# Performance work log

Hardware: AMD Instinct MI355X
Metric: run time of the kernel (lower is better)

The kernel has to match this reference:

```python
import jax, jax.numpy as jnp
import numpy as np

D_MODEL = 2048
N_HEADS = 16
HEAD_DIM = 128
WINDOW = 512
ROPE_BASE = 10000.0
B, N = 2, 2048
INNER = N_HEADS * HEAD_DIM


def setup_inputs() -> dict:
    key = jax.random.key(0)
    k1, k2, k3 = jax.random.split(key, 3)
    x = jax.random.normal(k1, (B, N, D_MODEL), dtype=jnp.float32)
    # torch nn.Linear stores weight as [out_features, in_features]
    w_qkv = jax.random.normal(k2, (3 * INNER, D_MODEL), dtype=jnp.float32) / np.sqrt(D_MODEL)
    w_o = jax.random.normal(k3, (D_MODEL, INNER), dtype=jnp.float32) / np.sqrt(INNER)
    return {"x": x, "w_qkv": w_qkv, "w_o": w_o}


def _rotate_half(t):
    t1, t2 = jnp.split(t, 2, axis=-1)
    return jnp.concatenate([-t2, t1], axis=-1)


def _rope(q, k, offset=0):
    # q, k: [B, H, N, D]; GPT-NeoX half-split rotary embedding
    D = q.shape[-1]
    inv_freq = 1.0 / (ROPE_BASE ** (jnp.arange(0, D, 2, dtype=jnp.float32) / D))
    pos = jnp.arange(q.shape[2], dtype=jnp.float32) + offset
    ang = pos[:, None] * inv_freq[None, :]                 # [N, D/2]
    cos = jnp.concatenate([jnp.cos(ang), jnp.cos(ang)], axis=-1)  # [N, D]
    sin = jnp.concatenate([jnp.sin(ang), jnp.sin(ang)], axis=-1)
    q_r = q * cos + _rotate_half(q) * sin
    k_r = k * cos + _rotate_half(k) * sin
    return q_r, k_r


def reference(x, w_qkv, w_o):
    Bq, Nq, _ = x.shape
    # QKV projection (no bias)
    qkv = jnp.einsum('bnd,ed->bne', x, w_qkv)              # [B, N, 3*INNER]
    q, k, v = jnp.split(qkv, 3, axis=-1)
    def to_heads(t):
        return t.reshape(Bq, Nq, N_HEADS, HEAD_DIM).transpose(0, 2, 1, 3)  # [B,H,N,D]
    q, k, v = to_heads(q), to_heads(k), to_heads(v)
    q, k = _rope(q, k, offset=0)
    # sliding-window causal mask: valid key j for query i iff (i - WINDOW) < j <= i
    i = jnp.arange(Nq)[:, None]
    j = jnp.arange(Nq)[None, :]
    valid = (j > i - WINDOW) & (j <= i)                    # [N, N]
    scale = 1.0 / np.sqrt(HEAD_DIM)
    scores = jnp.einsum('bhnd,bhkd->bhnk', q, k) * scale   # [B,H,N,N]
    scores = jnp.where(valid[None, None], scores, -jnp.inf)
    att = jax.nn.softmax(scores, axis=-1)
    out = jnp.einsum('bhnk,bhkd->bhnd', att, v)
    out = out.transpose(0, 2, 1, 3).reshape(Bq, Nq, INNER)
    y = jnp.einsum('bni,di->bnd', out, w_o)
    return y
```

## Files before the change

### kernel.cpp

```cpp
#include <hip/hip_runtime.h>
#include <hip/hip_bf16.h>
#include <cstdint>

typedef __bf16 bf16x8 __attribute__((ext_vector_type(8)));
typedef float floatx4 __attribute__((ext_vector_type(4)));

__device__ __forceinline__ void gl2lds16(const void* g, void* l) {
  __builtin_amdgcn_global_load_lds(
      (const __attribute__((address_space(1))) unsigned int*)g,
      (__attribute__((address_space(3))) unsigned int*)(uintptr_t)l,
      16, 0, 0);
}

__global__ __launch_bounds__(256)
void cvt_kernel(const float* __restrict__ in, __hip_bfloat16* __restrict__ out, int n) {
  int i = (blockIdx.x * 256 + threadIdx.x) * 4;
  if (i >= n) return;
  const float4 v = *(const float4*)(in + i);
  out[i + 0] = __float2bfloat16(v.x);
  out[i + 1] = __float2bfloat16(v.y);
  out[i + 2] = __float2bfloat16(v.z);
  out[i + 3] = __float2bfloat16(v.w);
}

__global__ __launch_bounds__(256)
void cvt2_kernel(const float* __restrict__ in0, const float* __restrict__ in1,
                 __hip_bfloat16* __restrict__ out, int n0, int ntot) {
  int i = (blockIdx.x * 256 + threadIdx.x) * 4;
  if (i >= ntot) return;
  const float4 v = (i < n0) ? *(const float4*)(in0 + i)
                            : *(const float4*)(in1 + (i - n0));
  out[i + 0] = __float2bfloat16(v.x);
  out[i + 1] = __float2bfloat16(v.y);
  out[i + 2] = __float2bfloat16(v.z);
  out[i + 3] = __float2bfloat16(v.w);
}

#define MEMFENCE asm volatile("" ::: "memory")

__global__ __launch_bounds__(256, 3)
void gemm_qkv128(const __hip_bfloat16* __restrict__ A,
                 const __hip_bfloat16* __restrict__ W,
                 __hip_bfloat16* __restrict__ Qr,
                 __hip_bfloat16* __restrict__ Kr,
                 __hip_bfloat16* __restrict__ Vt)
{
  extern __shared__ __hip_bfloat16 sm[];
  const int tid = threadIdx.x, lane = tid & 63, wave = tid >> 6;
  const int wr = wave >> 1, wc = wave & 1;
  const int bid = blockIdx.y * 32 + blockIdx.x;
  const int swz = (bid & 7) * 192 + (bid >> 3);
  const int m0 = (swz & 31) << 7;
  const int n0 = (swz >> 5) << 7;
  const int lrow = lane & 15, dg = lane >> 4, lq4 = dg * 4;
  const int rslot = (dg ^ ((lrow >> 1) & 3)) * 8;
  const int arow = tid >> 2;
  const int ascol = ((tid & 3) ^ ((tid >> 3) & 3)) * 8;
  const __hip_bfloat16* aS0 = A + (size_t)(m0 + arow) * 2048 + ascol;
  const __hip_bfloat16* aS1 = A + (size_t)(m0 + 64 + arow) * 2048 + ascol;
  const __hip_bfloat16* bS0 = W + (size_t)(n0 + arow) * 2048 + ascol;
  const __hip_bfloat16* bS1 = W + (size_t)(n0 + 64 + arow) * 2048 + ascol;
  float* invfp = (float*)((char*)sm + 49152);
  if (tid < 64) invfp[tid] = __expf(-(float)tid * 0.14391156831212787f);
  floatx4 acc[4][4] = {};

#define QS128(TT) do { const int bo_ = ((TT) % 3) * 8192; const int kk_ = (TT) * 32; \
    gl2lds16(aS0 + kk_, &sm[bo_ + tid * 8]);                                   \
    gl2lds16(aS1 + kk_, &sm[bo_ + 2048 + tid * 8]);                            \
    gl2lds16(bS0 + kk_, &sm[bo_ + 4096 + tid * 8]);                            \
    gl2lds16(bS1 + kk_, &sm[bo_ + 6144 + tid * 8]); } while (0)

#define QC128(BO) do {                                                         \
    bf16x8 af[4], bfr[4];                                                      \
    _Pragma("unroll")                                                          \
    for (int mt = 0; mt < 4; mt++)                                             \
      af[mt] = *(const bf16x8*)&sm[(BO) + (wr * 64 + mt * 16 + lrow) * 32 + rslot]; \
    _Pragma("unroll")                                                          \
    for (int nt = 0; nt < 4; nt++)                                             \
      bfr[nt] = *(const bf16x8*)&sm[(BO) + 4096 + (wc * 64 + nt * 16 + lrow) * 32 + rslot]; \
    __builtin_amdgcn_s_setprio(1);                                             \
    _Pragma("unroll")                                                          \
    for (int mt = 0; mt < 4; mt++)                                             \
      _Pragma("unroll")                                                        \
      for (int nt = 0; nt < 4; nt++)                                           \
        acc[mt][nt] = __builtin_amdgcn_mfma_f32_16x16x32_bf16(af[mt], bfr[nt], acc[mt][nt], 0, 0, 0); \
    __builtin_amdgcn_s_setprio(0);                                             \
  } while (0)

  QS128(0); QS128(1);
  for (int t = 0; t < 63; ++t) {
    MEMFENCE; __builtin_amdgcn_s_waitcnt(0x0074); MEMFENCE;
    __builtin_amdgcn_s_barrier(); MEMFENCE;
    if (t < 62) QS128(t + 2);
    QC128((t % 3) * 8192);
  }
  MEMFENCE; __builtin_amdgcn_s_waitcnt(0x0070); MEMFENCE;
  __builtin_amdgcn_s_barrier(); MEMFENCE;
  QC128((63 % 3) * 8192);
#undef QC128
#undef QS128

  const int seg = n0 >> 11;
  const int h = (n0 & 2047) >> 7;
  const int b = m0 >> 11;
  const int seq0 = m0 & 2047;
  __syncthreads();
  if (seg < 2) {
#pragma unroll
    for (int mt = 0; mt < 4; mt++)
#pragma unroll
      for (int nt = 0; nt < 4; nt++)
#pragma unroll
        for (int r = 0; r < 4; r++)
          sm[(wr * 64 + mt * 16 + lq4 + r) * 136 + wc * 64 + nt * 16 + lrow] =
              __float2bfloat16(acc[mt][nt][r]);
  } else {
#pragma unroll
    for (int mt = 0; mt < 4; mt++)
#pragma unroll
      for (int nt = 0; nt < 4; nt++)
#pragma unroll
        for (int r = 0; r < 4; r++)
          sm[(wc * 64 + nt * 16 + lrow) * 136 + wr * 64 + mt * 16 + lq4 + r] =
              __float2bfloat16(acc[mt][nt][r]);
  }
  __syncthreads();
  const float qs = (seg == 0) ? 0.08838834764831845f : 1.0f;
  if (seg < 2) {
    __hip_bfloat16* Out = seg ? Kr : Qr;
#pragma unroll
    for (int it = 0; it < 4; ++it) {
      const int task = tid + it * 256;
      const int row = task >> 3;
      const int g8 = (task & 7) * 8;
      const int seq = seq0 + row;
      const float pos = (float)seq;
      const bf16x8 lo8 = *(const bf16x8*)&sm[row * 136 + g8];
      const bf16x8 hi8 = *(const bf16x8*)&sm[row * 136 + g8 + 64];
      alignas(16) __hip_bfloat16 lo[8], hi[8];
#pragma unroll
      for (int k = 0; k < 8; k++) {
        float sn, cs;
        __sincosf(pos * invfp[g8 + k], &sn, &cs);
        const float a = (float)lo8[k];
        const float bb2 = (float)hi8[k];
        lo[k] = __float2bfloat16((a * cs - bb2 * sn) * qs);
        hi[k] = __float2bfloat16((bb2 * cs + a * sn) * qs);
      }
      const size_t ob = ((size_t)((b * 16 + h) * 2048 + seq)) * 128;
      *(bf16x8*)&Out[ob + g8] = *(const bf16x8*)lo;
      *(bf16x8*)&Out[ob + g8 + 64] = *(const bf16x8*)hi;
    }
  } else {
#pragma unroll
    for (int it = 0; it < 8; ++it) {
      const int task = tid + it * 256;
      const int col = task >> 4;
      const int sg = (task & 15) * 8;
      const bf16x8 v8 = *(const bf16x8*)&sm[col * 136 + sg];
      *(bf16x8*)&Vt[((size_t)((b * 16 + h) * 128 + col)) * 2048 + seq0 + sg] = v8;
    }
  }
}

__global__ __launch_bounds__(512, 2)
void gemm_o256(const __hip_bfloat16* __restrict__ A,
               const __hip_bfloat16* __restrict__ Wo,
               float* __restrict__ C)
{
  extern __shared__ __hip_bfloat16 sm[];
  const int tid = threadIdx.x, lane = tid & 63, wave = tid >> 6;
  const int wr = wave >> 2, wc = wave & 3;
  const int m0 = blockIdx.x << 8, n0 = blockIdx.y << 7;
  const int lrow = lane & 15, dg = lane >> 4, lq4 = dg * 4;
  const int rslot = (dg ^ ((lrow >> 1) & 3)) * 8;
  const int arow = tid >> 2;
  const int ascol = ((tid & 3) ^ ((tid >> 3) & 3)) * 8;
  const __hip_bfloat16* aS0 = A + (size_t)(m0 + arow) * 2048 + ascol;
  const __hip_bfloat16* aS1 = A + (size_t)(m0 + 128 + arow) * 2048 + ascol;
  const __hip_bfloat16* bS0 = Wo + (size_t)(n0 + arow) * 2048 + ascol;
  floatx4 acc[8][2] = {};

#define OSTAGE(TT) do { const int bb_ = (TT) & 3; const int kk_ = (TT) * 32;   \
    gl2lds16(aS0 + kk_, &sm[bb_ * 12288 + tid * 8]);                           \
    gl2lds16(aS1 + kk_, &sm[bb_ * 12288 + 4096 + tid * 8]);                    \
    gl2lds16(bS0 + kk_, &sm[bb_ * 12288 + 8192 + tid * 8]); } while (0)

#define OKSTEP(TT, WIMM, DOSTAGE) do {                                         \
    MEMFENCE; __builtin_amdgcn_s_waitcnt(WIMM); MEMFENCE;                      \
    __builtin_amdgcn_s_barrier(); MEMFENCE;                                    \
    const int bb = (TT) & 3;                                                   \
    if (DOSTAGE) OSTAGE((TT) + 3);                                             \
    bf16x8 af[8], bfr[2];                                                      \
    _Pragma("unroll")                                                          \
    for (int mt = 0; mt < 8; mt++)                                             \
      af[mt] = *(const bf16x8*)&sm[bb * 12288 + (wr * 128 + mt * 16 + lrow) * 32 + rslot]; \
    _Pragma("unroll")                                                          \
    for (int nt = 0; nt < 2; nt++)                                             \
      bfr[nt] = *(const bf16x8*)&sm[bb * 12288 + 8192 + (wc * 32 + nt * 16 + lrow) * 32 + rslot]; \
    __builtin_amdgcn_s_setprio(1);                                             \
    _Pragma("unroll")                                                          \
    for (int mt = 0; mt < 8; mt++)                                             \
      _Pragma("unroll")                                                        \
      for (int nt = 0; nt < 2; nt++)                                           \
        acc[mt][nt] = __builtin_amdgcn_mfma_f32_16x16x32_bf16(af[mt], bfr[nt], acc[mt][nt], 0, 0, 0); \
    __builtin_amdgcn_s_setprio(0);                                             \
  } while (0)

  OSTAGE(0); OSTAGE(1); OSTAGE(2);
  for (int t = 0; t < 61; ++t) OKSTEP(t, 0x0076, true);
  OKSTEP(61, 0x0076, false);
  OKSTEP(62, 0x0073, false);
  OKSTEP(63, 0x0070, false);
#undef OKSTEP
#undef OSTAGE

#pragma unroll
  for (int mt = 0; mt < 8; mt++)
#pragma unroll
    for (int nt = 0; nt < 2; nt++)
#pragma unroll
      for (int r = 0; r < 4; r++)
        C[(size_t)(m0 + wr * 128 + mt * 16 + lq4 + r) * 2048 +
          (n0 + wc * 32 + nt * 16 + lrow)] = acc[mt][nt][r];
}

#define KSTR 136
#define VSTR 72
__global__ __launch_bounds__(512, 4)
void attn_swa(const __hip_bfloat16* __restrict__ Qr, const __hip_bfloat16* __restrict__ Kr,
              const __hip_bfloat16* __restrict__ Vt, __hip_bfloat16* __restrict__ Out)
{
  __shared__ __hip_bfloat16 Ks[64 * KSTR];
  __shared__ __hip_bfloat16 Vs[128 * VSTR];
  __shared__ __hip_bfloat16 Pb[8][16 * VSTR];
  const int qt = blockIdx.x, bh = blockIdx.y;
  const int tid = threadIdx.x, lane = tid & 63, wave = tid >> 6;
  const int lrow = lane & 15, lk = (lane >> 4) * 8, lq4 = (lane >> 4) * 4;
  const int i0 = qt * 128;
  const float NEG_INF = -__builtin_inff();
  const __hip_bfloat16* Qh = Qr + (size_t)bh * 2048 * 128;
  const __hip_bfloat16* Kh = Kr + (size_t)bh * 2048 * 128;
  const __hip_bfloat16* Vh = Vt + (size_t)bh * 128 * 2048;

  const int ck0 = tid, ck1 = tid + 512;
  const int kr0 = ck0 >> 4, kg0 = (ck0 & 15) * 8;
  const int kr1 = ck1 >> 4, kg1 = (ck1 & 15) * 8;
  const int cv0 = tid, cv1 = tid + 512;
  const int vd0 = cv0 >> 3, vc0 = (cv0 & 7) * 8;
  const int vd1 = cv1 >> 3, vc1 = (cv1 & 7) * 8;

  const int iw = i0 + wave * 16 + lrow;
  bf16x8 qf[4];
#pragma unroll
  for (int ks = 0; ks < 4; ks++)
    qf[ks] = *(const bf16x8*)&Qh[(size_t)iw * 128 + ks * 32 + lk];

  floatx4 accO[8] = {};
  float m_i = NEG_INF, l_i = 0.f;
  const int imin = i0 + wave * 16;
  const int lo = i0 - 511;
  const int jt_lo = (lo > 0 ? lo : 0) >> 6;
  const int jt_hi = (i0 + 127) >> 6;

  int j0n = jt_lo * 64;
  int4 rk0 = *(const int4*)&Kh[(size_t)(j0n + kr0) * 128 + kg0];
  int4 rk1 = *(const int4*)&Kh[(size_t)(j0n + kr1) * 128 + kg1];
  int4 rv0 = *(const int4*)&Vh[(size_t)vd0 * 2048 + j0n + vc0];
  int4 rv1 = *(const int4*)&Vh[(size_t)vd1 * 2048 + j0n + vc1];

  for (int jt = jt_lo; jt <= jt_hi; jt++) {
    const int j0 = jt * 64;
    __syncthreads();
    *(int4*)&Ks[kr0 * KSTR + kg0] = rk0;
    *(int4*)&Ks[kr1 * KSTR + kg1] = rk1;
    *(int4*)&Vs[vd0 * VSTR + vc0] = rv0;
    *(int4*)&Vs[vd1 * VSTR + vc1] = rv1;
    if (jt < jt_hi) {
      const int jn = j0 + 64;
      rk0 = *(const int4*)&Kh[(size_t)(jn + kr0) * 128 + kg0];
      rk1 = *(const int4*)&Kh[(size_t)(jn + kr1) * 128 + kg1];
      rv0 = *(const int4*)&Vh[(size_t)vd0 * 2048 + jn + vc0];
      rv1 = *(const int4*)&Vh[(size_t)vd1 * 2048 + jn + vc1];
    }
    asm volatile("" ::: "memory");
    __builtin_amdgcn_s_waitcnt(0xC07F);
    __builtin_amdgcn_s_barrier();
    asm volatile("" ::: "memory");

    floatx4 s[4] = {};
#pragma unroll
    for (int nt = 0; nt < 4; nt++) {
      const int krow = (nt * 16 + lrow) * KSTR;
#pragma unroll
      for (int ks = 0; ks < 4; ks++) {
        const bf16x8 kf = *(const bf16x8*)&Ks[krow + ks * 32 + lk];
        s[nt] = __builtin_amdgcn_mfma_f32_16x16x32_bf16(kf, qf[ks], s[nt], 0, 0, 0);
      }
    }
    const bool full = (j0 + 63 <= imin) && (j0 >= imin + 15 - 511);
    float rmax = NEG_INF;
    if (full) {
#pragma unroll
      for (int nt = 0; nt < 4; nt++)
#pragma unroll
        for (int r = 0; r < 4; r++) rmax = fmaxf(rmax, s[nt][r]);
    } else {
#pragma unroll
      for (int nt = 0; nt < 4; nt++) {
#pragma unroll
        for (int r = 0; r < 4; r++) {
          const int j = j0 + nt * 16 + lq4 + r;
          const float sv = ((j <= iw) && (j > iw - 512)) ? s[nt][r] : NEG_INF;
          s[nt][r] = sv;
          rmax = fmaxf(rmax, sv);
        }
      }
    }
    rmax = fmaxf(rmax, __shfl_xor(rmax, 16));
    rmax = fmaxf(rmax, __shfl_xor(rmax, 32));
    const float mnew = fmaxf(m_i, rmax);
    const float alpha = __expf(fminf(m_i - mnew, 0.f));
    m_i = mnew;
    float rs = 0.f;
    if (full) {
#pragma unroll
      for (int nt = 0; nt < 4; nt++)
#pragma unroll
        for (int r = 0; r < 4; r++) {
          const float p = __expf(s[nt][r] - mnew);
          s[nt][r] = p;
          rs += p;
        }
    } else {
#pragma unroll
      for (int nt = 0; nt < 4; nt++)
#pragma unroll
        for (int r = 0; r < 4; r++) {
          const float sv = s[nt][r];
          const float p = (sv == NEG_INF) ? 0.f : __expf(sv - mnew);
          s[nt][r] = p;
          rs += p;
        }
    }
    rs += __shfl_xor(rs, 16);
    rs += __shfl_xor(rs, 32);
    l_i = l_i * alpha + rs;
#pragma unroll
    for (int dt = 0; dt < 8; dt++) accO[dt] *= alpha;
#pragma unroll
    for (int nt = 0; nt < 4; nt++) {
      alignas(8) __hip_bfloat16 p4[4];
#pragma unroll
      for (int r = 0; r < 4; r++) p4[r] = __float2bfloat16(s[nt][r]);
      *(uint64_t*)&Pb[wave][lrow * VSTR + nt * 16 + lq4] = *(const uint64_t*)p4;
    }
    bf16x8 pf[2];
#pragma unroll
    for (int jf = 0; jf < 2; jf++)
      pf[jf] = *(const bf16x8*)&Pb[wave][lrow * VSTR + jf * 32 + lk];
#pragma unroll
    for (int dt = 0; dt < 8; dt++) {
      const int vrow = (dt * 16 + lrow) * VSTR;
#pragma unroll
      for (int jf = 0; jf < 2; jf++) {
        const bf16x8 vf = *(const bf16x8*)&Vs[vrow + jf * 32 + lk];
        accO[dt] = __builtin_amdgcn_mfma_f32_16x16x32_bf16(vf, pf[jf], accO[dt], 0, 0, 0);
      }
    }
  }
  const int b = bh >> 4, h = bh & 15;
  const float inv_l = 1.0f / l_i;
  const size_t rowb = ((size_t)(b * 2048 + iw)) * 2048 + h * 128;
#pragma unroll
  for (int dt = 0; dt < 8; dt++) {
    alignas(8) __hip_bfloat16 o4[4];
#pragma unroll
    for (int r = 0; r < 4; r++) o4[r] = __float2bfloat16(accO[dt][r] * inv_l);
    *(uint64_t*)&Out[rowb + dt * 16 + lq4] = *(const uint64_t*)o4;
  }
}

extern "C" void kernel_launch(void* const* d_in, const int* in_sizes, int n_in,
                              void* d_out, int out_size, void* d_ws, size_t ws_size,
                              hipStream_t stream)
{
  const float* x = (const float*)d_in[0];
  const float* w_qkv = (const float*)d_in[1];
  const float* w_o = (const float*)d_in[2];
  float* y = (float*)d_out;
  char* ws = (char*)d_ws;

  const size_t SZ_X = 16777216;
  const size_t SZ_WQKV = 25165824;
  const size_t SZ_Q = 16777216;

  __hip_bfloat16* xb = (__hip_bfloat16*)(ws);
  __hip_bfloat16* wqkvb = (__hip_bfloat16*)(ws + SZ_X);
  __hip_bfloat16* Qr = (__hip_bfloat16*)(ws + SZ_X + SZ_WQKV);
  __hip_bfloat16* Kr = (__hip_bfloat16*)(ws + SZ_X + SZ_WQKV + SZ_Q);
  __hip_bfloat16* Vt = (__hip_bfloat16*)(ws + SZ_X + SZ_WQKV + 2 * SZ_Q);

  static bool s_attr_done = false;
  if (!s_attr_done) {
    hipFuncSetAttribute((const void*)gemm_o256,
                        hipFuncAttributeMaxDynamicSharedMemorySize, 98304);
    s_attr_done = true;
  }

  cvt2_kernel<<<dim3(20480), dim3(256), 0, stream>>>(x, w_qkv, xb, 8388608, 20971520);
  gemm_qkv128<<<dim3(32, 48), dim3(256), 49408, stream>>>(xb, wqkvb, Qr, Kr, Vt);
  attn_swa<<<dim3(16, 32), dim3(512), 0, stream>>>(Qr, Kr, Vt, xb );
  cvt_kernel<<<dim3(4096), dim3(256), 0, stream>>>(w_o, wqkvb, 4194304);
  gemm_o256<<<dim3(16, 16), dim3(512), 98304, stream>>>(xb, wqkvb, y);
}
```

Measured before the change: 357.9 us.

## Enlarge QKV GEMM tile to 256x128 with 512-thread blocks

Reworks the QKV projection GEMM from 128x128 tiles on 256 threads to 256x128 tiles on 512 threads (8 waves arranged 4x2). The LDS staging buffers, the load pattern, the grid swizzle and the epilogue transpose strides are all updated to match. Each block now reuses every weight tile across twice as many rows, which cuts global and L2 traffic for W. The cost is more shared memory per block (about 74KB) and a grid of half as many blocks, which may reduce occupancy and tail balance.

```diff
diff --git a/kernel.cpp b/kernel.cpp
--- a/kernel.cpp
+++ b/kernel.cpp
@@ -38,46 +38,44 @@
 
 #define MEMFENCE asm volatile("" ::: "memory")
 
-__global__ __launch_bounds__(256, 3)
-void gemm_qkv128(const __hip_bfloat16* __restrict__ A,
-                 const __hip_bfloat16* __restrict__ W,
-                 __hip_bfloat16* __restrict__ Qr,
-                 __hip_bfloat16* __restrict__ Kr,
-                 __hip_bfloat16* __restrict__ Vt)
+__global__ __launch_bounds__(512, 4)
+void gemm_qkvA(const __hip_bfloat16* __restrict__ A,
+               const __hip_bfloat16* __restrict__ W,
+               __hip_bfloat16* __restrict__ Qr,
+               __hip_bfloat16* __restrict__ Kr,
+               __hip_bfloat16* __restrict__ Vt)
 {
   extern __shared__ __hip_bfloat16 sm[];
   const int tid = threadIdx.x, lane = tid & 63, wave = tid >> 6;
   const int wr = wave >> 1, wc = wave & 1;
-  const int bid = blockIdx.y * 32 + blockIdx.x;
-  const int swz = (bid & 7) * 192 + (bid >> 3);
-  const int m0 = (swz & 31) << 7;
-  const int n0 = (swz >> 5) << 7;
+  const int idx = blockIdx.y * 16 + blockIdx.x;
+  const int swz = (idx & 7) * 96 + (idx >> 3);
+  const int m0 = (swz & 15) << 8;
+  const int n0 = (swz >> 4) << 7;
   const int lrow = lane & 15, dg = lane >> 4, lq4 = dg * 4;
   const int rslot = (dg ^ ((lrow >> 1) & 3)) * 8;
   const int arow = tid >> 2;
   const int ascol = ((tid & 3) ^ ((tid >> 3) & 3)) * 8;
   const __hip_bfloat16* aS0 = A + (size_t)(m0 + arow) * 2048 + ascol;
-  const __hip_bfloat16* aS1 = A + (size_t)(m0 + 64 + arow) * 2048 + ascol;
+  const __hip_bfloat16* aS1 = A + (size_t)(m0 + 128 + arow) * 2048 + ascol;
   const __hip_bfloat16* bS0 = W + (size_t)(n0 + arow) * 2048 + ascol;
-  const __hip_bfloat16* bS1 = W + (size_t)(n0 + 64 + arow) * 2048 + ascol;
-  float* invfp = (float*)((char*)sm + 49152);
+  float* invfp = (float*)((char*)sm + 73728);
   if (tid < 64) invfp[tid] = __expf(-(float)tid * 0.14391156831212787f);
   floatx4 acc[4][4] = {};
 
-#define QS128(TT) do { const int bo_ = ((TT) % 3) * 8192; const int kk_ = (TT) * 32; \
+#define ASTG(TT) do { const int bo_ = ((TT) % 3) * 12288; const int kk_ = (TT) * 32; \
     gl2lds16(aS0 + kk_, &sm[bo_ + tid * 8]);                                   \
-    gl2lds16(aS1 + kk_, &sm[bo_ + 2048 + tid * 8]);                            \
-    gl2lds16(bS0 + kk_, &sm[bo_ + 4096 + tid * 8]);                            \
-    gl2lds16(bS1 + kk_, &sm[bo_ + 6144 + tid * 8]); } while (0)
-
-#define QC128(BO) do {                                                         \
+    gl2lds16(aS1 + kk_, &sm[bo_ + 4096 + tid * 8]);                            \
+    gl2lds16(bS0 + kk_, &sm[bo_ + 8192 + tid * 8]); } while (0)
+
+#define ACOMP(BO) do {                                                         \
     bf16x8 af[4], bfr[4];                                                      \
     _Pragma("unroll")                                                          \
     for (int mt = 0; mt < 4; mt++)                                             \
       af[mt] = *(const bf16x8*)&sm[(BO) + (wr * 64 + mt * 16 + lrow) * 32 + rslot]; \
     _Pragma("unroll")                                                          \
     for (int nt = 0; nt < 4; nt++)                                             \
-      bfr[nt] = *(const bf16x8*)&sm[(BO) + 4096 + (wc * 64 + nt * 16 + lrow) * 32 + rslot]; \
+      bfr[nt] = *(const bf16x8*)&sm[(BO) + 8192 + (wc * 64 + nt * 16 + lrow) * 32 + rslot]; \
     __builtin_amdgcn_s_setprio(1);                                             \
     _Pragma("unroll")                                                          \
     for (int mt = 0; mt < 4; mt++)                                             \
@@ -87,18 +85,18 @@
     __builtin_amdgcn_s_setprio(0);                                             \
   } while (0)
 
-  QS128(0); QS128(1);
+  ASTG(0); ASTG(1);
   for (int t = 0; t < 63; ++t) {
-    MEMFENCE; __builtin_amdgcn_s_waitcnt(0x0074); MEMFENCE;
+    MEMFENCE; __builtin_amdgcn_s_waitcnt(0x0073); MEMFENCE;
     __builtin_amdgcn_s_barrier(); MEMFENCE;
-    if (t < 62) QS128(t + 2);
-    QC128((t % 3) * 8192);
+    if (t < 62) ASTG(t + 2);
+    ACOMP((t % 3) * 12288);
   }
   MEMFENCE; __builtin_amdgcn_s_waitcnt(0x0070); MEMFENCE;
   __builtin_amdgcn_s_barrier(); MEMFENCE;
-  QC128((63 % 3) * 8192);
-#undef QC128
-#undef QS128
+  ACOMP((63 % 3) * 12288);
+#undef ACOMP
+#undef ASTG
 
   const int seg = n0 >> 11;
   const int h = (n0 & 2047) >> 7;
@@ -121,7 +119,7 @@
       for (int nt = 0; nt < 4; nt++)
 #pragma unroll
         for (int r = 0; r < 4; r++)
-          sm[(wc * 64 + nt * 16 + lrow) * 136 + wr * 64 + mt * 16 + lq4 + r] =
+          sm[(wc * 64 + nt * 16 + lrow) * 264 + wr * 64 + mt * 16 + lq4 + r] =
               __float2bfloat16(acc[mt][nt][r]);
   }
   __syncthreads();
@@ -130,7 +128,7 @@
     __hip_bfloat16* Out = seg ? Kr : Qr;
 #pragma unroll
     for (int it = 0; it < 4; ++it) {
-      const int task = tid + it * 256;
+      const int task = tid + it * 512;
       const int row = task >> 3;
       const int g8 = (task & 7) * 8;
       const int seq = seq0 + row;
@@ -154,10 +152,10 @@
   } else {
 #pragma unroll
     for (int it = 0; it < 8; ++it) {
-      const int task = tid + it * 256;
-      const int col = task >> 4;
-      const int sg = (task & 15) * 8;
-      const bf16x8 v8 = *(const bf16x8*)&sm[col * 136 + sg];
+      const int task = tid + it * 512;
+      const int col = task >> 5;
+      const int sg = (task & 31) * 8;
+      const bf16x8 v8 = *(const bf16x8*)&sm[col * 264 + sg];
       *(bf16x8*)&Vt[((size_t)((b * 16 + h) * 128 + col)) * 2048 + seq0 + sg] = v8;
     }
   }
@@ -403,13 +401,15 @@
 
   static bool s_attr_done = false;
   if (!s_attr_done) {
+    hipFuncSetAttribute((const void*)gemm_qkvA,
+                        hipFuncAttributeMaxDynamicSharedMemorySize, 73984);
     hipFuncSetAttribute((const void*)gemm_o256,
                         hipFuncAttributeMaxDynamicSharedMemorySize, 98304);
     s_attr_done = true;
   }
 
   cvt2_kernel<<<dim3(20480), dim3(256), 0, stream>>>(x, w_qkv, xb, 8388608, 20971520);
-  gemm_qkv128<<<dim3(32, 48), dim3(256), 49408, stream>>>(xb, wqkvb, Qr, Kr, Vt);
+  gemm_qkvA<<<dim3(16, 48), dim3(512), 73984, stream>>>(xb, wqkvb, Qr, Kr, Vt);
   attn_swa<<<dim3(16, 32), dim3(512), 0, stream>>>(Qr, Kr, Vt, xb );
   cvt_kernel<<<dim3(4096), dim3(256), 0, stream>>>(w_o, wqkvb, 4194304);
   gemm_o256<<<dim3(16, 16), dim3(512), 98304, stream>>>(xb, wqkvb, y);
```

New measurement: 340.5 us. 4.9% less time.
